# Performance work log

Measured on AMD Instinct MI355X. Metric: run time of the kernel, lower is better.

Reference implementation:

```python
import jax, jax.numpy as jnp
import numpy as np

SAI, B, CK, H, W = 9, 4, 64, 32, 32
CV = 64
RADIUS = 4.0 / 8.0  # valid_dis_range / 8


def setup_inputs() -> dict:
    key = jax.random.key(0)
    k1, k2, k3, k4, k5 = jax.random.split(key, 5)
    return {
        "memory_keys": jax.random.normal(k1, (SAI, B, CK, H, W), dtype=jnp.float32),
        "memory_values": jax.random.normal(k2, (SAI, B, CV, H, W), dtype=jnp.float32),
        "query_query": jax.random.normal(k3, (B, CK, H, W), dtype=jnp.float32),
        "disparity": jax.random.normal(k4, (B, 1, H, W), dtype=jnp.float32),
        "sequence_index": jax.random.randint(k5, (B, SAI, 2), 0, 11, dtype=jnp.int32),
    }


def reference(memory_keys, memory_values, query_query, disparity, sequence_index):
    sai, b, ck, h, w = memory_keys.shape
    cv = memory_values.shape[2]
    shw = sai * h * w

    # keys: (sai,b,ck,h,w) -> (b, ck, sai*h*w)
    keys = jnp.transpose(memory_keys, (1, 2, 0, 3, 4)).reshape(b, ck, shw)
    # query: (b, ck, h*w) -> (b, h*w, ck)
    q = query_query.reshape(b, ck, h * w).transpose(0, 2, 1)
    # scores: (b, h*w, sai*h*w)
    scores = jnp.einsum("bqc,bck->bqk", q, keys)

    # distance-based additive mask (per batch, per frame, per key pixel)
    seq = sequence_index.astype(jnp.float32)
    dist = jnp.sqrt((seq[:, :, 1] - 5.0) ** 2 + (seq[:, :, 0] - 5.0) ** 2)  # (b, sai)
    # total_disparity: (b, sai, h, w); disparity is (b,1,h,w)
    total = dist[:, :, None, None] * disparity
    large = jnp.abs(total) > RADIUS  # mask==1 where |disp| exceeds radius
    # bias: 0 where mask==1, -inf where mask==0 (per original masked_fill)
    bias = jnp.where(large, 0.0, -jnp.inf).reshape(b, 1, shw)

    scores = scores + bias  # broadcasts over query positions
    attn = jax.nn.softmax(scores, axis=-1)

    # values: (sai,b,cv,h,w) -> (b, sai*h*w, cv)
    vals = jnp.transpose(memory_values, (1, 2, 0, 3, 4)).reshape(b, cv, shw).transpose(0, 2, 1)
    mem = jnp.einsum("bqk,bkc->bqc", attn, vals)  # (b, h*w, cv)
    return mem.transpose(0, 2, 1).reshape(b, cv, h, w)
```

## Files before the change

### kernel.cpp

```cpp
#include <hip/hip_runtime.h>
#include <math.h>

#define SAI 9
#define NB  4
#define CK  64
#define CV  64
#define HW  1024
#define QT  32
#define RSW 136
#define RSTR 68

typedef __attribute__((ext_vector_type(8))) short bf16x8;
typedef __attribute__((ext_vector_type(4))) float f32x4;
typedef unsigned short u16;
typedef unsigned int u32;

__device__ __forceinline__ u16 f2bf(float x) {
    unsigned u = __float_as_uint(x);
    return (u16)((u + 0x7fff + ((u >> 16) & 1)) >> 16);
}
__device__ __forceinline__ float bf2f(u16 s) {
    return __uint_as_float(((unsigned)s) << 16);
}
__device__ __forceinline__ unsigned pk2(float a, float b) {
    return (unsigned)f2bf(a) | ((unsigned)f2bf(b) << 16);
}
__device__ __forceinline__ void lds_barrier() {
    __asm__ __volatile__("s_waitcnt lgkmcnt(0)\n\ts_barrier" ::: "memory");
}

__global__ __launch_bounds__(256) void cfa_prep(
    const float* __restrict__ keys, const float* __restrict__ vals,
    u16* __restrict__ khi, u16* __restrict__ vbf)
{
    const int gid = blockIdx.x * 256 + threadIdx.x;
    const int isV = gid >= (SAI * NB * 8192);
    const int id  = isV ? gid - SAI * NB * 8192 : gid;
    const int f   = id >> 13;
    const int r   = id & 8191;
    const int lane = r & 63;
    const int gg   = r >> 6;
    const int l15 = lane & 15, quad = lane >> 4;
    const size_t fb = (size_t)f * (64 * 1024);

    if (!isV) {
        const int p  = (gg >> 1) * 16 + l15;
        const int c0 = (gg & 1) * 32 + quad * 8;
        const float* src = keys + fb + (size_t)c0 * HW + p;
        float x[8];
#pragma unroll
        for (int j = 0; j < 8; ++j) x[j] = src[(size_t)j * HW];
        uint4 ph;
        u32* php = (u32*)&ph;
#pragma unroll
        for (int h2 = 0; h2 < 4; ++h2)
            php[h2] = pk2(x[h2 * 2], x[h2 * 2 + 1]);
        *(uint4*)&khi[fb + (size_t)gg * 512 + lane * 8] = ph;
    } else {
        const int p = (gg >> 2) * 32 + quad * 8;
        const int c = (gg & 3) * 16 + l15;
        const float* src = vals + fb + (size_t)c * HW + p;
        const float4 a = *(const float4*)src;
        const float4 b = *(const float4*)(src + 4);
        uint4 pv;
        pv.x = pk2(a.x, a.y); pv.y = pk2(a.z, a.w);
        pv.z = pk2(b.x, b.y); pv.w = pk2(b.z, b.w);
        *(uint4*)&vbf[fb + (size_t)gg * 512 + lane * 8] = pv;
    }
}

__global__ __launch_bounds__(256, 4) void cfa_main(
    const u16* __restrict__ khi, const u16* __restrict__ vbf,
    const float* __restrict__ query, const float* __restrict__ disp,
    const int* __restrict__ seq,
    float* __restrict__ numW, float* __restrict__ denW)
{
    __shared__ alignas(16) u16 sW[2][QT * RSW];
    __shared__ float sDen[4 * QT];

    const int tid = threadIdx.x;
    const int w = tid >> 6;
    const int lane = tid & 63;
    const int l15 = lane & 15, quad = lane >> 4;
    const int f  = blockIdx.x % 36;
    const int qt = blockIdx.x / 36;
    const int s  = f / NB;
    const int b  = f % NB;
    const int p0 = qt * QT;
    const size_t fb = (size_t)f * (64 * 1024);

    const float d0 = (float)seq[(b * SAI + s) * 2 + 0] - 5.f;
    const float d1 = (float)seq[(b * SAI + s) * 2 + 1] - 5.f;
    const float dist = sqrtf(d0 * d0 + d1 * d1);

    bf16x8 qh[2][2], ql[2][2];
#pragma unroll
    for (int q2 = 0; q2 < 2; ++q2)
#pragma unroll
        for (int ks = 0; ks < 2; ++ks)
#pragma unroll
            for (int j = 0; j < 8; ++j) {
                float x = query[(size_t)(b * CK + ks * 32 + quad * 8 + j) * HW + p0 + q2 * 16 + l15];
                u16 h = f2bf(x);
                qh[q2][ks][j] = (short)h;
                ql[q2][ks][j] = (short)f2bf(x - bf2f(h));
            }

    f32x4 acc[2];
#pragma unroll
    for (int q2 = 0; q2 < 2; ++q2)
#pragma unroll
        for (int r = 0; r < 4; ++r) acc[q2][r] = 0.f;
    float den[2] = {0.f, 0.f};

    uint4 kbh[2][2];
#define LOADK(tt)                                                              \
    {                                                                          \
        _Pragma("unroll") for (int kt = 0; kt < 2; ++kt)                       \
        _Pragma("unroll") for (int ks = 0; ks < 2; ++ks) {                     \
            const size_t ka = fb +                                             \
                (size_t)((((tt) * 8 + w * 2 + kt) * 2) + ks) * 512 + lane * 8; \
            kbh[kt][ks] = *(const uint4*)&khi[ka];                             \
        }                                                                      \
    }

    LOADK(0);

    for (int t = 0; t < 8; ++t) {
        u16* const wbuf = sW[t & 1];

        uint4 vb[4];
#pragma unroll
        for (int k2 = 0; k2 < 4; ++k2)
            vb[k2] = *(const uint4*)&vbf[fb + (size_t)((t * 4 + k2) * 4 + w) * 512 + lane * 8];
        const float4 dv0 = *(const float4*)(disp + b * HW + t * 128 + w * 32 + quad * 4);
        const float4 dv1 = *(const float4*)(disp + b * HW + t * 128 + w * 32 + 16 + quad * 4);

        f32x4 sc[2][2];
#pragma unroll
        for (int q2 = 0; q2 < 2; ++q2)
#pragma unroll
            for (int kt = 0; kt < 2; ++kt)
#pragma unroll
                for (int r = 0; r < 4; ++r) sc[q2][kt][r] = 0.f;

#pragma unroll
        for (int kt = 0; kt < 2; ++kt)
#pragma unroll
            for (int ks = 0; ks < 2; ++ks) {
                const bf16x8 kh = __builtin_bit_cast(bf16x8, kbh[kt][ks]);
#pragma unroll
                for (int q2 = 0; q2 < 2; ++q2) {
                    sc[q2][kt] = __builtin_amdgcn_mfma_f32_16x16x32_bf16(kh, qh[q2][ks], sc[q2][kt], 0, 0, 0);
                    sc[q2][kt] = __builtin_amdgcn_mfma_f32_16x16x32_bf16(kh, ql[q2][ks], sc[q2][kt], 0, 0, 0);
                }
            }

#pragma unroll
        for (int kt = 0; kt < 2; ++kt) {
            const float4 dv = kt ? dv1 : dv0;
            const float m0 = (fabsf(dist * dv.x) > 0.5f) ? 1.f : 0.f;
            const float m1 = (fabsf(dist * dv.y) > 0.5f) ? 1.f : 0.f;
            const float m2 = (fabsf(dist * dv.z) > 0.5f) ? 1.f : 0.f;
            const float m3 = (fabsf(dist * dv.w) > 0.5f) ? 1.f : 0.f;
#pragma unroll
            for (int q2 = 0; q2 < 2; ++q2) {
                const float e0 = m0 * __expf(sc[q2][kt][0]);
                const float e1 = m1 * __expf(sc[q2][kt][1]);
                const float e2 = m2 * __expf(sc[q2][kt][2]);
                const float e3 = m3 * __expf(sc[q2][kt][3]);
                den[q2] += (e0 + e1) + (e2 + e3);
                uint2 pk;
                pk.x = pk2(e0, e1);
                pk.y = pk2(e2, e3);
                *(uint2*)&wbuf[(q2 * 16 + l15) * RSW + w * 32 + kt * 16 + quad * 4] = pk;
            }
        }

        LOADK((t + 1) & 7);

        lds_barrier();

#pragma unroll
        for (int k2 = 0; k2 < 4; ++k2) {
            const bf16x8 vf = __builtin_bit_cast(bf16x8, vb[k2]);
#pragma unroll
            for (int q2 = 0; q2 < 2; ++q2) {
                const bf16x8 wf = __builtin_bit_cast(bf16x8,
                    *(const uint4*)&wbuf[(q2 * 16 + l15) * RSW + k2 * 32 + quad * 8]);
                acc[q2] = __builtin_amdgcn_mfma_f32_16x16x32_bf16(wf, vf, acc[q2], 0, 0, 0);
            }
        }
    }
#undef LOADK

#pragma unroll
    for (int q2 = 0; q2 < 2; ++q2) {
        den[q2] += __shfl_xor(den[q2], 16, 64);
        den[q2] += __shfl_xor(den[q2], 32, 64);
    }
    if (quad == 0) {
#pragma unroll
        for (int q2 = 0; q2 < 2; ++q2)
            sDen[w * QT + q2 * 16 + l15] = den[q2];
    }
    __syncthreads();
    if (tid < QT)
        denW[(size_t)f * HW + p0 + tid] =
            sDen[tid] + sDen[QT + tid] + sDen[2 * QT + tid] + sDen[3 * QT + tid];

#pragma unroll
    for (int q2 = 0; q2 < 2; ++q2)
#pragma unroll
        for (int r = 0; r < 4; ++r) {
            const int q = q2 * 16 + quad * 4 + r;
            const int c = w * 16 + l15;
            numW[((size_t)f * HW + p0 + q) * CV + c] = acc[q2][r];
        }
}

__global__ __launch_bounds__(256) void cfa_reduce(
    const float* __restrict__ numW, const float* __restrict__ denW,
    float* __restrict__ out)
{
    const int tid = threadIdx.x;
    const int bid = blockIdx.x;
    const int b = bid >> 8;
    const int p = (bid & 255) * 4 + (tid >> 6);
    const int c = tid & 63;
    float num = 0.f, den = 0.f;
#pragma unroll
    for (int s = 0; s < SAI; ++s) {
        num += numW[(((size_t)(s * NB + b)) * HW + p) * CV + c];
        den += denW[((size_t)(s * NB + b)) * HW + p];
    }
    out[((size_t)b * CV + c) * HW + p] = num / den;
}

__global__ __launch_bounds__(256, 2) void cfa_fb(
    const float* __restrict__ keys, const float* __restrict__ vals,
    const float* __restrict__ query, const float* __restrict__ disp,
    const int* __restrict__ seq,
    float* __restrict__ numW, float* __restrict__ denW,
    float* __restrict__ out, int nS)
{
    __shared__ alignas(16) unsigned int sV[CV * RSTR];
    __shared__ alignas(16) unsigned int sWb[32 * RSTR];
    __shared__ float sDen[4 * 32];
    __shared__ float sDenTot[32];

    const int tid  = threadIdx.x;
    const int w    = tid >> 6;
    const int lane = tid & 63;
    const int l15  = lane & 15;
    const int quad = lane >> 4;
    const int b    = blockIdx.y;
    const int s0   = blockIdx.z;
    const int p0   = blockIdx.x * 32;
    const bool direct = (nS == SAI);

    bf16x8 qhi[2][2], qlo[2][2];
#pragma unroll
    for (int qt = 0; qt < 2; ++qt)
#pragma unroll
        for (int ks = 0; ks < 2; ++ks)
#pragma unroll
            for (int j = 0; j < 8; ++j) {
                float x = query[(size_t)(b * CK + ks * 32 + quad * 8 + j) * HW + p0 + qt * 16 + l15];
                u16 h = f2bf(x);
                qhi[qt][ks][j] = (short)h;
                qlo[qt][ks][j] = (short)f2bf(x - bf2f(h));
            }

    f32x4 acc[2];
#pragma unroll
    for (int qt = 0; qt < 2; ++qt)
#pragma unroll
        for (int r = 0; r < 4; ++r) acc[qt][r] = 0.f;
    float denacc[2][4] = {{0.f,0.f,0.f,0.f},{0.f,0.f,0.f,0.f}};

    for (int si = 0; si < nS; ++si) {
        const int s = s0 + si;
        const float d0 = (float)seq[(b * SAI + s) * 2 + 0] - 5.f;
        const float d1 = (float)seq[(b * SAI + s) * 2 + 1] - 5.f;
        const float dist = sqrtf(d0 * d0 + d1 * d1);
        const float* Kf = keys + (size_t)(s * NB + b) * CK * HW;
        const float* Vf = vals + (size_t)(s * NB + b) * CV * HW;

        for (int t = 0; t < HW / 128; ++t) {
            const int t128 = t * 128;
            __syncthreads();
#pragma unroll
            for (int it = 0; it < 4; ++it) {
                const int gidx = it * 256 + tid;
                const int c = gidx >> 4;
                const int g = gidx & 15;
                const float* vp = Vf + (size_t)c * HW + t128 + g * 8;
                const float4 f0 = *(const float4*)(vp);
                const float4 f1 = *(const float4*)(vp + 4);
                uint4 pk;
                pk.x = pk2(f0.x, f0.y); pk.y = pk2(f0.z, f0.w);
                pk.z = pk2(f1.x, f1.y); pk.w = pk2(f1.z, f1.w);
                *(uint4*)&sV[c * RSTR + g * 4] = pk;
            }

            f32x4 sc[2][2];
#pragma unroll
            for (int qt = 0; qt < 2; ++qt)
#pragma unroll
                for (int kt = 0; kt < 2; ++kt)
#pragma unroll
                    for (int r = 0; r < 4; ++r) sc[qt][kt][r] = 0.f;

            const int keyBase = t128 + w * 32 + l15;
#pragma unroll
            for (int kt = 0; kt < 2; ++kt)
#pragma unroll
                for (int ks = 0; ks < 2; ++ks) {
                    bf16x8 kh, kl;
#pragma unroll
                    for (int j = 0; j < 8; ++j) {
                        float x = Kf[(size_t)(ks * 32 + quad * 8 + j) * HW + keyBase + kt * 16];
                        u16 h = f2bf(x);
                        kh[j] = (short)h;
                        kl[j] = (short)f2bf(x - bf2f(h));
                    }
#pragma unroll
                    for (int qt = 0; qt < 2; ++qt) {
                        sc[qt][kt] = __builtin_amdgcn_mfma_f32_16x16x32_bf16(qhi[qt][ks], kh, sc[qt][kt], 0, 0, 0);
                        sc[qt][kt] = __builtin_amdgcn_mfma_f32_16x16x32_bf16(qhi[qt][ks], kl, sc[qt][kt], 0, 0, 0);
                        sc[qt][kt] = __builtin_amdgcn_mfma_f32_16x16x32_bf16(qlo[qt][ks], kh, sc[qt][kt], 0, 0, 0);
                    }
                }

#pragma unroll
            for (int kt = 0; kt < 2; ++kt) {
                const int kk = w * 32 + kt * 16 + l15;
                const float dvv = disp[b * HW + t128 + kk];
                const float msk = (fabsf(dist * dvv) > 0.5f) ? 1.f : 0.f;
#pragma unroll
                for (int qt = 0; qt < 2; ++qt)
#pragma unroll
                    for (int r = 0; r < 4; ++r) {
                        const float e = msk * __expf(sc[qt][kt][r]);
                        denacc[qt][r] += e;
                        const int q = qt * 16 + quad * 4 + r;
                        ((u16*)sWb)[q * (2 * RSTR) + kk] = f2bf(e);
                    }
            }
            __syncthreads();

            const int c = w * 16 + l15;
#pragma unroll
            for (int ks2 = 0; ks2 < 4; ++ks2) {
                const int g = ks2 * 4 + quad;
                uint4 vr = *(uint4*)&sV[c * RSTR + g * 4];
                bf16x8 vfrag = __builtin_bit_cast(bf16x8, vr);
#pragma unroll
                for (int qt = 0; qt < 2; ++qt) {
                    const int q = qt * 16 + l15;
                    uint4 wr = *(uint4*)&sWb[q * RSTR + g * 4];
                    bf16x8 wfrag = __builtin_bit_cast(bf16x8, wr);
                    acc[qt] = __builtin_amdgcn_mfma_f32_16x16x32_bf16(wfrag, vfrag, acc[qt], 0, 0, 0);
                }
            }
        }
    }

#pragma unroll
    for (int off = 1; off < 16; off <<= 1)
#pragma unroll
        for (int qt = 0; qt < 2; ++qt)
#pragma unroll
            for (int r = 0; r < 4; ++r)
                denacc[qt][r] += __shfl_xor(denacc[qt][r], off, 64);

    if (l15 == 0)
#pragma unroll
        for (int qt = 0; qt < 2; ++qt)
#pragma unroll
            for (int r = 0; r < 4; ++r)
                sDen[w * 32 + qt * 16 + quad * 4 + r] = denacc[qt][r];
    __syncthreads();

    if (tid < 32) {
        const float d = sDen[tid] + sDen[32 + tid] + sDen[64 + tid] + sDen[96 + tid];
        if (direct) sDenTot[tid] = d;
        else        denW[(size_t)(s0 * NB + b) * HW + p0 + tid] = d;
    }

    if (direct) {
        __syncthreads();
#pragma unroll
        for (int qt = 0; qt < 2; ++qt)
#pragma unroll
            for (int r = 0; r < 4; ++r) {
                const int q = qt * 16 + quad * 4 + r;
                const int c = w * 16 + l15;
                out[((size_t)b * CV + c) * HW + p0 + q] = acc[qt][r] / sDenTot[q];
            }
    } else {
#pragma unroll
        for (int qt = 0; qt < 2; ++qt)
#pragma unroll
            for (int r = 0; r < 4; ++r) {
                const int q = qt * 16 + quad * 4 + r;
                const int c = w * 16 + l15;
                numW[((size_t)(s0 * NB + b) * HW + p0 + q) * CV + c] = acc[qt][r];
            }
    }
}

extern "C" void kernel_launch(void* const* d_in, const int* in_sizes, int n_in,
                              void* d_out, int out_size, void* d_ws, size_t ws_size,
                              hipStream_t stream) {
    const float* keys  = (const float*)d_in[0];
    const float* vals  = (const float*)d_in[1];
    const float* query = (const float*)d_in[2];
    const float* disp  = (const float*)d_in[3];
    const int*   seq   = (const int*)d_in[4];
    float* out = (float*)d_out;

    const size_t numElems = (size_t)SAI * NB * HW * CV;
    const size_t denElems = (size_t)SAI * NB * HW;
    const size_t partBytes = (numElems + denElems) * sizeof(float);
    const size_t fragBytes = (size_t)SAI * NB * CK * HW * 2;
    const size_t needFull = partBytes + 2 * fragBytes;

    float* numW = (float*)d_ws;
    float* denW = numW + numElems;

    if (ws_size >= needFull) {
        u16* khi = (u16*)((char*)d_ws + partBytes);
        u16* vbf = (u16*)((char*)khi + fragBytes);
        hipLaunchKernelGGL(cfa_prep, dim3(2 * SAI * NB * 8192 / 256), dim3(256), 0, stream,
                           keys, vals, khi, vbf);
        hipLaunchKernelGGL(cfa_main, dim3(36 * (HW / QT)), dim3(256), 0, stream,
                           khi, vbf, query, disp, seq, numW, denW);
        hipLaunchKernelGGL(cfa_reduce, dim3(1024), dim3(256), 0, stream,
                           numW, denW, out);
    } else if (ws_size >= partBytes) {
        hipLaunchKernelGGL(cfa_fb, dim3(HW / 32, NB, SAI), dim3(256), 0, stream,
                           keys, vals, query, disp, seq, numW, denW, (float*)nullptr, 1);
        hipLaunchKernelGGL(cfa_reduce, dim3(1024), dim3(256), 0, stream,
                           numW, denW, out);
    } else {
        hipLaunchKernelGGL(cfa_fb, dim3(HW / 32, NB, 1), dim3(256), 0, stream,
                           keys, vals, query, disp, seq,
                           (float*)nullptr, (float*)nullptr, out, SAI);
    }
}
```

Measured before the change: 107.8 us.

## Double waves per block in cfa_main, splitting PV output across query halves

The main attention kernel moves from 4 to 8 wavefronts per block. Each wave computes scores for its own 32-key slice, so the key loop drops from 8 to 4 iterations. In the PV stage each wave now owns one 16-query by 16-channel output tile rather than two, which halves its accumulators and the LDS weight reads per wave. The aim is more parallelism and latency hiding per query tile. In exchange each wave issues twice as many V-fragment loads per iteration and uses more LDS per block, which could reduce occupancy.

Result: slower. 140.7 us (+30.6%).

```diff
diff --git a/kernel.cpp b/kernel.cpp
--- a/kernel.cpp
+++ b/kernel.cpp
@@ -7,7 +7,7 @@
 #define CV  64
 #define HW  1024
 #define QT  32
-#define RSW 136
+#define RSW2 264
 #define RSTR 68
 
 typedef __attribute__((ext_vector_type(8))) short bf16x8;
@@ -69,14 +69,14 @@
     }
 }
 
-__global__ __launch_bounds__(256, 4) void cfa_main(
+__global__ __launch_bounds__(512, 4) void cfa_main(
     const u16* __restrict__ khi, const u16* __restrict__ vbf,
     const float* __restrict__ query, const float* __restrict__ disp,
     const int* __restrict__ seq,
     float* __restrict__ numW, float* __restrict__ denW)
 {
-    __shared__ alignas(16) u16 sW[2][QT * RSW];
-    __shared__ float sDen[4 * QT];
+    __shared__ alignas(16) u16 sW[2][QT * RSW2];
+    __shared__ float sDen[8 * QT];
 
     const int tid = threadIdx.x;
     const int w = tid >> 6;
@@ -88,6 +88,8 @@
     const int b  = f % NB;
     const int p0 = qt * QT;
     const size_t fb = (size_t)f * (64 * 1024);
+    const int cg  = w & 3;
+    const int qh2 = w >> 2;
 
     const float d0 = (float)seq[(b * SAI + s) * 2 + 0] - 5.f;
     const float d1 = (float)seq[(b * SAI + s) * 2 + 1] - 5.f;
@@ -106,11 +108,9 @@
                 ql[q2][ks][j] = (short)f2bf(x - bf2f(h));
             }
 
-    f32x4 acc[2];
-#pragma unroll
-    for (int q2 = 0; q2 < 2; ++q2)
-#pragma unroll
-        for (int r = 0; r < 4; ++r) acc[q2][r] = 0.f;
+    f32x4 acc;
+#pragma unroll
+    for (int r = 0; r < 4; ++r) acc[r] = 0.f;
     float den[2] = {0.f, 0.f};
 
     uint4 kbh[2][2];
@@ -119,22 +119,22 @@
         _Pragma("unroll") for (int kt = 0; kt < 2; ++kt)                       \
         _Pragma("unroll") for (int ks = 0; ks < 2; ++ks) {                     \
             const size_t ka = fb +                                             \
-                (size_t)((((tt) * 8 + w * 2 + kt) * 2) + ks) * 512 + lane * 8; \
+                (size_t)((((tt) * 16 + w * 2 + kt) * 2) + ks) * 512 + lane * 8;\
             kbh[kt][ks] = *(const uint4*)&khi[ka];                             \
         }                                                                      \
     }
 
     LOADK(0);
 
-    for (int t = 0; t < 8; ++t) {
+    for (int t = 0; t < 4; ++t) {
         u16* const wbuf = sW[t & 1];
 
-        uint4 vb[4];
-#pragma unroll
-        for (int k2 = 0; k2 < 4; ++k2)
-            vb[k2] = *(const uint4*)&vbf[fb + (size_t)((t * 4 + k2) * 4 + w) * 512 + lane * 8];
-        const float4 dv0 = *(const float4*)(disp + b * HW + t * 128 + w * 32 + quad * 4);
-        const float4 dv1 = *(const float4*)(disp + b * HW + t * 128 + w * 32 + 16 + quad * 4);
+        uint4 vb[8];
+#pragma unroll
+        for (int k2 = 0; k2 < 8; ++k2)
+            vb[k2] = *(const uint4*)&vbf[fb + (size_t)((t * 8 + k2) * 4 + cg) * 512 + lane * 8];
+        const float4 dv0 = *(const float4*)(disp + b * HW + t * 256 + w * 32 + quad * 4);
+        const float4 dv1 = *(const float4*)(disp + b * HW + t * 256 + w * 32 + 16 + quad * 4);
 
         f32x4 sc[2][2];
 #pragma unroll
@@ -173,23 +173,20 @@
                 uint2 pk;
                 pk.x = pk2(e0, e1);
                 pk.y = pk2(e2, e3);
-                *(uint2*)&wbuf[(q2 * 16 + l15) * RSW + w * 32 + kt * 16 + quad * 4] = pk;
+                *(uint2*)&wbuf[(q2 * 16 + l15) * RSW2 + w * 32 + kt * 16 + quad * 4] = pk;
             }
         }
 
-        LOADK((t + 1) & 7);
+        LOADK((t + 1) & 3);
 
         lds_barrier();
 
 #pragma unroll
-        for (int k2 = 0; k2 < 4; ++k2) {
+        for (int k2 = 0; k2 < 8; ++k2) {
             const bf16x8 vf = __builtin_bit_cast(bf16x8, vb[k2]);
-#pragma unroll
-            for (int q2 = 0; q2 < 2; ++q2) {
-                const bf16x8 wf = __builtin_bit_cast(bf16x8,
-                    *(const uint4*)&wbuf[(q2 * 16 + l15) * RSW + k2 * 32 + quad * 8]);
-                acc[q2] = __builtin_amdgcn_mfma_f32_16x16x32_bf16(wf, vf, acc[q2], 0, 0, 0);
-            }
+            const bf16x8 wf = __builtin_bit_cast(bf16x8,
+                *(const uint4*)&wbuf[(qh2 * 16 + l15) * RSW2 + k2 * 32 + quad * 8]);
+            acc = __builtin_amdgcn_mfma_f32_16x16x32_bf16(wf, vf, acc, 0, 0, 0);
         }
     }
 #undef LOADK
@@ -205,18 +202,19 @@
             sDen[w * QT + q2 * 16 + l15] = den[q2];
     }
     __syncthreads();
-    if (tid < QT)
-        denW[(size_t)f * HW + p0 + tid] =
-            sDen[tid] + sDen[QT + tid] + sDen[2 * QT + tid] + sDen[3 * QT + tid];
-
-#pragma unroll
-    for (int q2 = 0; q2 < 2; ++q2)
-#pragma unroll
-        for (int r = 0; r < 4; ++r) {
-            const int q = q2 * 16 + quad * 4 + r;
-            const int c = w * 16 + l15;
-            numW[((size_t)f * HW + p0 + q) * CV + c] = acc[q2][r];
-        }
+    if (tid < QT) {
+        float dsum = 0.f;
+#pragma unroll
+        for (int ww = 0; ww < 8; ++ww) dsum += sDen[ww * QT + tid];
+        denW[(size_t)f * HW + p0 + tid] = dsum;
+    }
+
+#pragma unroll
+    for (int r = 0; r < 4; ++r) {
+        const int q = qh2 * 16 + quad * 4 + r;
+        const int c = cg * 16 + l15;
+        numW[((size_t)f * HW + p0 + q) * CV + c] = acc[r];
+    }
 }
 
 __global__ __launch_bounds__(256) void cfa_reduce(
@@ -435,7 +433,7 @@
         u16* vbf = (u16*)((char*)khi + fragBytes);
         hipLaunchKernelGGL(cfa_prep, dim3(2 * SAI * NB * 8192 / 256), dim3(256), 0, stream,
                            keys, vals, khi, vbf);
-        hipLaunchKernelGGL(cfa_main, dim3(36 * (HW / QT)), dim3(256), 0, stream,
+        hipLaunchKernelGGL(cfa_main, dim3(36 * (HW / QT)), dim3(512), 0, stream,
                            khi, vbf, query, disp, seq, numW, denW);
         hipLaunchKernelGGL(cfa_reduce, dim3(1024), dim3(256), 0, stream,
                            numW, denW, out);
```
